# Kernel tuning notes

Measured on AMD Instinct MI355X. Metric: run time of the kernel, lower is better.

## Reference

```python
import jax, jax.numpy as jnp
import numpy as np

COMMITMENT_COST = 0.25


def setup_inputs() -> dict:
    key = jax.random.key(0)
    k1, k2 = jax.random.split(key)
    B, H, W, D, K = 64, 32, 32, 64, 1024
    x = jax.random.normal(k1, (B, H, W, D), dtype=jnp.float32)
    # variance_scaling(fan_in=D, uniform) ~ U(-sqrt(3/D), sqrt(3/D)); plain normal*scale is fine for a reference
    embeddings = jax.random.uniform(k2, (D, K), dtype=jnp.float32,
                                    minval=-np.sqrt(3.0 / D), maxval=np.sqrt(3.0 / D))
    return {"x": x, "embeddings": embeddings}


def reference(x, embeddings):
    D = embeddings.shape[0]
    K = embeddings.shape[1]
    flat = x.reshape(-1, D)                                   # [N, D]
    # squared euclidean distance: ||f||^2 - 2 f.E + ||e||^2 -> [N, K]
    distance = (jnp.sum(flat ** 2, axis=1, keepdims=True)
                - 2.0 * jnp.matmul(flat, embeddings)
                + jnp.sum(embeddings ** 2, axis=0, keepdims=True))
    encoding_indices_flat = jnp.argmax(-distance, axis=1)     # [N]
    encodings = jax.nn.one_hot(encoding_indices_flat, K, dtype=distance.dtype)  # [N, K]
    encoding_indices = encoding_indices_flat.reshape(x.shape[:-1])
    # quantize: gather rows of E^T -> same shape as x
    quantized = jnp.take(embeddings.T, encoding_indices, axis=0)
    e_latent_loss = jnp.mean((jax.lax.stop_gradient(quantized) - x) ** 2)
    q_latent_loss = jnp.mean((quantized - jax.lax.stop_gradient(x)) ** 2)
    loss = q_latent_loss + COMMITMENT_COST * e_latent_loss
    quantized_st = x + jax.lax.stop_gradient(quantized - x)   # straight-through
    avg_probs = jnp.mean(encodings, axis=0)                   # [K]
    perplexity = jnp.exp(-jnp.sum(avg_probs * jnp.log(avg_probs + 1e-10)))
    return quantized_st, loss, perplexity, encoding_indices
```

## Files before the change

### kernel.cpp

```cpp
#include <hip/hip_runtime.h>
#include <math.h>


typedef __attribute__((ext_vector_type(8))) short short8v;
typedef __attribute__((ext_vector_type(4))) float float4v;
typedef unsigned short u16;
typedef unsigned int u32;

constexpr int D = 64;
constexpr int K = 1024;
constexpr int NPTS = 65536;
constexpr long QOFF = (long)NPTS * D;
constexpr float BIAS = 24.0f;
constexpr float GATE = 5e-3f;

constexpr size_t OFF_LOSS = 0;
constexpr size_t OFF_CNT  = 256;
constexpr size_t OFF_EC   = OFF_CNT + 4096;
constexpr size_t OFF_ECB  = OFF_EC + 4096;
constexpr size_t OFF_ET   = OFF_ECB + 4096;
constexpr size_t OFF_STG  = OFF_ET + (size_t)K * D * 4;

__device__ __forceinline__ float med3(float a, float b, float c) {
  return __builtin_amdgcn_fmed3f(a, b, c);
}
__device__ __forceinline__ u16 bf16rtn(float x) {
  u32 u = __float_as_uint(x);
  return (u16)((u + 0x7fffu + ((u >> 16) & 1u)) >> 16);
}
__device__ __forceinline__ float bf2f(u16 h) {
  return __uint_as_float(((u32)h) << 16);
}
__device__ __forceinline__ void gl_lds16(const void* g, void* l) {
  __builtin_amdgcn_global_load_lds(
      (const __attribute__((address_space(1))) u32*)g,
      (__attribute__((address_space(3))) u32*)l, 16, 0, 0);
}

__global__ __launch_bounds__(256) void vq_conv(const float* __restrict__ E,
                                               float* __restrict__ Et,
                                               unsigned char* __restrict__ stg) {
  int gid = blockIdx.x * 256 + threadIdx.x;
  int k = gid & 1023;
  int dg = gid >> 10;
  float v[4];
#pragma unroll
  for (int i = 0; i < 4; ++i) v[i] = E[(dg * 4 + i) * K + k];
  *(float4*)&Et[(size_t)k * 64 + dg * 4] = make_float4(v[0], v[1], v[2], v[3]);
  u16 h[4], l[4];
#pragma unroll
  for (int i = 0; i < 4; ++i) {
    float m2 = -2.0f * v[i];
    h[i] = bf16rtn(m2);
    l[i] = bf16rtn(m2 - bf2f(h[i]));
  }
  int s = dg >> 3, q = (dg >> 1) & 3, jb = (dg & 1) * 4;
  size_t base = (size_t)(k >> 4) * 4096 + (size_t)s * 1024 +
                (size_t)((q * 16 + (k & 15)) * 16) + (size_t)(jb * 2);
  ushort4 hv = {h[0], h[1], h[2], h[3]};
  ushort4 lv = {l[0], l[1], l[2], l[3]};
  *(ushort4*)&stg[base] = hv;
  *(ushort4*)&stg[base + 2048] = lv;
}

__global__ __launch_bounds__(256) void vq_norm(const float* __restrict__ E,
                                               float* __restrict__ eC,
                                               float* __restrict__ eCb,
                                               double* __restrict__ lossSum,
                                               int* __restrict__ counts) {
  int k = blockIdx.x * 256 + threadIdx.x;
  float c = __fmul_rn(E[k], E[k]);
#pragma unroll
  for (int d = 1; d < D; ++d) {
    float vv = E[d * K + k];
    c = __fadd_rn(c, __fmul_rn(vv, vv));
  }
  eC[k] = c;
  eCb[k] = c + BIAS;
  counts[k] = 0;
  if (k == 0) *lossSum = 0.0;
}

__global__ __launch_bounds__(256) void vq_main(const float* __restrict__ x,
                                               const unsigned char* __restrict__ stg,
                                               const float* __restrict__ eC,
                                               const float* __restrict__ eCb,
                                               const float* __restrict__ Etg,
                                               float* __restrict__ out,
                                               double* __restrict__ lossSum,
                                               int* __restrict__ counts) {
  __shared__ __align__(16) unsigned char sbuf[4][2][8192];
  __shared__ __align__(16) float ecb[1024];
  __shared__ __align__(16) float topbuf[256 * 4];
  __shared__ int bkbuf[128];

  const int tid = threadIdx.x;
  const int w = tid >> 6;
  const int lane = tid & 63;
  const int col = lane & 15;
  const int quad = lane >> 4;
  const int blockBase = blockIdx.x * 128;
  const float INF = __builtin_inff();

  *(float4*)&ecb[tid * 4] = *(const float4*)&eCb[tid * 4];

  short8v Bh[2][2], Bl[2][2];
#pragma unroll
  for (int pt = 0; pt < 2; ++pt) {
    const float* xp = x + (size_t)(blockBase + w * 32 + pt * 16 + col) * 64;
#pragma unroll
    for (int s = 0; s < 2; ++s) {
      const float4* src = (const float4*)(xp + s * 32 + quad * 8);
      float4 a = src[0], b = src[1];
      float xs[8] = {a.x, a.y, a.z, a.w, b.x, b.y, b.z, b.w};
      short8v hf, lf;
#pragma unroll
      for (int j = 0; j < 8; ++j) {
        u16 h = bf16rtn(xs[j]);
        hf[j] = (short)h;
        lf[j] = (short)bf16rtn(xs[j] - bf2f(h));
      }
      Bh[pt][s] = hf;
      Bl[pt][s] = lf;
    }
  }

  {
    const unsigned char* s0 = stg + (size_t)lane * 16;
#pragma unroll
    for (int i = 0; i < 8; ++i)
      gl_lds16(s0 + i * 1024, &sbuf[w][0][i * 1024 + lane * 16]);
#pragma unroll
    for (int i = 0; i < 8; ++i)
      gl_lds16(s0 + 8192 + i * 1024, &sbuf[w][1][i * 1024 + lane * 16]);
  }
  asm volatile("s_waitcnt lgkmcnt(0)" ::: "memory");
  __builtin_amdgcn_s_barrier();
  __builtin_amdgcn_sched_barrier(0);
  asm volatile("" ::: "memory");

  float b1[2] = {INF, INF}, b2[2] = {INF, INF};

#pragma unroll 1
  for (int ch = 0; ch < 32; ++ch) {
    const unsigned char* bufB = sbuf[w][ch & 1];
    if (ch < 31) {
      asm volatile("s_waitcnt vmcnt(8)" ::: "memory");
    } else {
      asm volatile("s_waitcnt vmcnt(0)" ::: "memory");
    }
#pragma unroll
    for (int ct2 = 0; ct2 < 2; ++ct2) {
      const unsigned char* fb = bufB + ct2 * 4096 + lane * 16;
      short8v Ah0 = *(const short8v*)(fb);
      short8v Ah1 = *(const short8v*)(fb + 1024);
      short8v Al0 = *(const short8v*)(fb + 2048);
      short8v Al1 = *(const short8v*)(fb + 3072);
      float4v Ci = *(const float4v*)&ecb[ch * 32 + ct2 * 16 + quad * 4];
#pragma unroll
      for (int pt = 0; pt < 2; ++pt) {
        float4v Ca = Ci;
        float4v Cb = {0.f, 0.f, 0.f, 0.f};
        Ca = __builtin_amdgcn_mfma_f32_16x16x32_bf16(Ah0, Bh[pt][0], Ca, 0, 0, 0);
        Cb = __builtin_amdgcn_mfma_f32_16x16x32_bf16(Ah1, Bh[pt][1], Cb, 0, 0, 0);
        Ca = __builtin_amdgcn_mfma_f32_16x16x32_bf16(Al0, Bh[pt][0], Ca, 0, 0, 0);
        Cb = __builtin_amdgcn_mfma_f32_16x16x32_bf16(Al1, Bh[pt][1], Cb, 0, 0, 0);
        Ca = __builtin_amdgcn_mfma_f32_16x16x32_bf16(Ah0, Bl[pt][0], Ca, 0, 0, 0);
        Cb = __builtin_amdgcn_mfma_f32_16x16x32_bf16(Ah1, Bl[pt][1], Cb, 0, 0, 0);
#pragma unroll
        for (int r = 0; r < 4; ++r) {
          float dv = Ca[r] + Cb[r];
          u32 u = (__float_as_uint(dv) & 0xffffff00u) |
                  (u32)(ch * 8 + ct2 * 4 + r);
          float v = __uint_as_float(u);
          float pb = b1[pt];
          b1[pt] = fminf(pb, v);
          b2[pt] = med3(pb, b2[pt], v);
        }
      }
    }
    asm volatile("s_waitcnt lgkmcnt(0)" ::: "memory");
    if (ch < 30) {
      const unsigned char* s2 = stg + (size_t)(ch + 2) * 8192 + (size_t)lane * 16;
#pragma unroll
      for (int i = 0; i < 8; ++i)
        gl_lds16(s2 + i * 1024, &sbuf[w][ch & 1][i * 1024 + lane * 16]);
    }
  }

  topbuf[tid * 4 + 0] = b1[0];
  topbuf[tid * 4 + 1] = b2[0];
  topbuf[tid * 4 + 2] = b1[1];
  topbuf[tid * 4 + 3] = b2[1];
  __syncthreads();

  if (tid < 128) {
    const int mw = tid >> 5, mpt = (tid >> 4) & 1, mcol = tid & 15;
    float cv[8];
    int cq[8];
    float mv0 = INF, mv1 = INF;
    int q0 = 0;
#pragma unroll
    for (int q = 0; q < 4; ++q) {
      int lbase = (mw * 64 + q * 16 + mcol) * 4 + mpt * 2;
#pragma unroll
      for (int j = 0; j < 2; ++j) {
        float v = topbuf[lbase + j];
        cv[q * 2 + j] = v;
        cq[q * 2 + j] = q;
        if (v < mv0) { mv1 = mv0; mv0 = v; q0 = q; }
        else if (v < mv1) { mv1 = v; }
      }
    }
    u32 lb = __float_as_uint(mv0) & 255u;
    int bestk = (int)((lb >> 3) * 32 + ((lb >> 2) & 1) * 16 + q0 * 4 + (lb & 3));

    if (mv1 - mv0 < GATE) {
      const float* f = x + (size_t)(blockBase + tid) * 64;
      float r8[8];
#pragma unroll
      for (int j = 0; j < 8; ++j) { float fv = f[j]; r8[j] = __fmul_rn(fv, fv); }
#pragma unroll
      for (int i = 8; i < D; i += 8)
#pragma unroll
        for (int j = 0; j < 8; ++j) {
          float fv = f[i + j];
          r8[j] = __fadd_rn(r8[j], __fmul_rn(fv, fv));
        }
      float A = __fadd_rn(__fadd_rn(__fadd_rn(r8[0], r8[1]), __fadd_rn(r8[2], r8[3])),
                          __fadd_rn(__fadd_rn(r8[4], r8[5]), __fadd_rn(r8[6], r8[7])));
      float bd = INF;
      int bkk = K;
#pragma unroll
      for (int c = 0; c < 8; ++c) {
        u32 cb = __float_as_uint(cv[c]) & 255u;
        int k = (int)((cb >> 3) * 32 + ((cb >> 2) & 1) * 16 + cq[c] * 4 + (cb & 3));
        const float* er = Etg + (size_t)k * 64;
        float m = 0.f;
#pragma unroll
        for (int d = 0; d < D; ++d) m = __fmaf_rn(f[d], er[d], m);
        float dist = __fadd_rn(__fsub_rn(A, __fmul_rn(2.f, m)), eC[k]);
        bool better = (dist < bd) || (dist == bd && k < bkk);
        bd = better ? dist : bd;
        bkk = better ? k : bkk;
      }
      bestk = bkk;
    }

    bkbuf[tid] = bestk;
    out[QOFF + 2 + blockBase + tid] = (float)bestk;
    atomicAdd(&counts[bestk], 1);
  }
  __syncthreads();

  const int pp = tid >> 1, half = tid & 1;
  const int bk = bkbuf[pp];
  const float4* et = (const float4*)(Etg + (size_t)bk * 64 + half * 32);
  const float4* xr = (const float4*)(x + (size_t)(blockBase + pp) * 64 + half * 32);
  float4* ov = (float4*)(out + (size_t)(blockBase + pp) * 64 + half * 32);
  float errs = 0.f;
#pragma unroll
  for (int i = 0; i < 8; ++i) {
    float4 qv = et[i];
    float4 xv = xr[i];
    float dx;
    dx = qv.x - xv.x; errs = fmaf(dx, dx, errs);
    dx = qv.y - xv.y; errs = fmaf(dx, dx, errs);
    dx = qv.z - xv.z; errs = fmaf(dx, dx, errs);
    dx = qv.w - xv.w; errs = fmaf(dx, dx, errs);
    ov[i] = qv;
  }
  double de = (double)errs;
#pragma unroll
  for (int off = 32; off > 0; off >>= 1) de += __shfl_down(de, off, 64);
  if (lane == 0) atomicAdd(lossSum, de);
}

__global__ __launch_bounds__(256) void vq_finalize(const double* __restrict__ lossSum,
                                                   const int* __restrict__ counts,
                                                   float* __restrict__ out) {
  __shared__ double sh[256];
  double ent = 0.0;
  for (int k = threadIdx.x; k < K; k += 256) {
    double pp = (double)counts[k] / (double)NPTS;
    ent += pp * log(pp + 1e-10);
  }
  sh[threadIdx.x] = ent;
  __syncthreads();
  for (int s = 128; s > 0; s >>= 1) {
    if (threadIdx.x < s) sh[threadIdx.x] += sh[threadIdx.x + s];
    __syncthreads();
  }
  if (threadIdx.x == 0) {
    out[QOFF + 0] = (float)(1.25 * (*lossSum) / (double)((long)NPTS * D));
    out[QOFF + 1] = (float)exp(-sh[0]);
  }
}

extern "C" void kernel_launch(void* const* d_in, const int* in_sizes, int n_in,
                              void* d_out, int out_size, void* d_ws, size_t ws_size,
                              hipStream_t stream) {
  const float* x = (const float*)d_in[0];
  const float* E = (const float*)d_in[1];
  float* out = (float*)d_out;

  char* ws = (char*)d_ws;
  double* lossSum = (double*)(ws + OFF_LOSS);
  int* counts = (int*)(ws + OFF_CNT);
  float* eC = (float*)(ws + OFF_EC);
  float* eCb = (float*)(ws + OFF_ECB);
  float* Etg = (float*)(ws + OFF_ET);
  unsigned char* stgb = (unsigned char*)(ws + OFF_STG);

  vq_conv<<<64, 256, 0, stream>>>(E, Etg, stgb);
  vq_norm<<<4, 256, 0, stream>>>(E, eC, eCb, lossSum, counts);
  vq_main<<<NPTS / 128, 256, 0, stream>>>(x, stgb, eC, eCb, Etg, out,
                                          lossSum, counts);
  vq_finalize<<<1, 256, 0, stream>>>(lossSum, counts, out);
}
```

Measured before the change: 130.4 us.

## Halve points per wave and codebook chunk size to raise occupancy

Each wave now handles 16 points instead of 32, and each staged codebook chunk holds 16 codes (4 KB) instead of 32, so the loop runs 64 iterations instead of 32. The grid doubles to 1024 blocks, LDS per block shrinks, and launch_bounds requests 4 blocks per CU. The aim is more resident waves and better latency hiding. In exchange, every staged codebook chunk is reused across half as many points, so total global/LDS traffic for the codebook doubles and there are more loop iterations and waits per MFMA.

```diff
diff --git a/kernel.cpp b/kernel.cpp
--- a/kernel.cpp
+++ b/kernel.cpp
@@ -81,33 +81,32 @@
   if (k == 0) *lossSum = 0.0;
 }
 
-__global__ __launch_bounds__(256) void vq_main(const float* __restrict__ x,
-                                               const unsigned char* __restrict__ stg,
-                                               const float* __restrict__ eC,
-                                               const float* __restrict__ eCb,
-                                               const float* __restrict__ Etg,
-                                               float* __restrict__ out,
-                                               double* __restrict__ lossSum,
-                                               int* __restrict__ counts) {
-  __shared__ __align__(16) unsigned char sbuf[4][2][8192];
+__global__ __launch_bounds__(256, 4) void vq_main(const float* __restrict__ x,
+                                                  const unsigned char* __restrict__ stg,
+                                                  const float* __restrict__ eC,
+                                                  const float* __restrict__ eCb,
+                                                  const float* __restrict__ Etg,
+                                                  float* __restrict__ out,
+                                                  double* __restrict__ lossSum,
+                                                  int* __restrict__ counts) {
+  __shared__ __align__(16) unsigned char sbuf[4][2][4096];
   __shared__ __align__(16) float ecb[1024];
-  __shared__ __align__(16) float topbuf[256 * 4];
-  __shared__ int bkbuf[128];
+  __shared__ __align__(16) float topbuf[256 * 2];
+  __shared__ int bkbuf[64];
 
   const int tid = threadIdx.x;
   const int w = tid >> 6;
   const int lane = tid & 63;
   const int col = lane & 15;
   const int quad = lane >> 4;
-  const int blockBase = blockIdx.x * 128;
+  const int blockBase = blockIdx.x * 64;
   const float INF = __builtin_inff();
 
   *(float4*)&ecb[tid * 4] = *(const float4*)&eCb[tid * 4];
 
-  short8v Bh[2][2], Bl[2][2];
-#pragma unroll
-  for (int pt = 0; pt < 2; ++pt) {
-    const float* xp = x + (size_t)(blockBase + w * 32 + pt * 16 + col) * 64;
+  short8v Bh[2], Bl[2];
+  {
+    const float* xp = x + (size_t)(blockBase + w * 16 + col) * 64;
 #pragma unroll
     for (int s = 0; s < 2; ++s) {
       const float4* src = (const float4*)(xp + s * 32 + quad * 8);
@@ -120,89 +119,80 @@
         hf[j] = (short)h;
         lf[j] = (short)bf16rtn(xs[j] - bf2f(h));
       }
-      Bh[pt][s] = hf;
-      Bl[pt][s] = lf;
+      Bh[s] = hf;
+      Bl[s] = lf;
     }
   }
 
   {
     const unsigned char* s0 = stg + (size_t)lane * 16;
 #pragma unroll
-    for (int i = 0; i < 8; ++i)
+    for (int i = 0; i < 4; ++i)
       gl_lds16(s0 + i * 1024, &sbuf[w][0][i * 1024 + lane * 16]);
 #pragma unroll
-    for (int i = 0; i < 8; ++i)
-      gl_lds16(s0 + 8192 + i * 1024, &sbuf[w][1][i * 1024 + lane * 16]);
+    for (int i = 0; i < 4; ++i)
+      gl_lds16(s0 + 4096 + i * 1024, &sbuf[w][1][i * 1024 + lane * 16]);
   }
   asm volatile("s_waitcnt lgkmcnt(0)" ::: "memory");
   __builtin_amdgcn_s_barrier();
   __builtin_amdgcn_sched_barrier(0);
   asm volatile("" ::: "memory");
 
-  float b1[2] = {INF, INF}, b2[2] = {INF, INF};
+  float b1 = INF, b2 = INF;
 
 #pragma unroll 1
-  for (int ch = 0; ch < 32; ++ch) {
+  for (int ch = 0; ch < 64; ++ch) {
     const unsigned char* bufB = sbuf[w][ch & 1];
-    if (ch < 31) {
-      asm volatile("s_waitcnt vmcnt(8)" ::: "memory");
+    if (ch < 63) {
+      asm volatile("s_waitcnt vmcnt(4)" ::: "memory");
     } else {
       asm volatile("s_waitcnt vmcnt(0)" ::: "memory");
     }
-#pragma unroll
-    for (int ct2 = 0; ct2 < 2; ++ct2) {
-      const unsigned char* fb = bufB + ct2 * 4096 + lane * 16;
-      short8v Ah0 = *(const short8v*)(fb);
-      short8v Ah1 = *(const short8v*)(fb + 1024);
-      short8v Al0 = *(const short8v*)(fb + 2048);
-      short8v Al1 = *(const short8v*)(fb + 3072);
-      float4v Ci = *(const float4v*)&ecb[ch * 32 + ct2 * 16 + quad * 4];
-#pragma unroll
-      for (int pt = 0; pt < 2; ++pt) {
-        float4v Ca = Ci;
-        float4v Cb = {0.f, 0.f, 0.f, 0.f};
-        Ca = __builtin_amdgcn_mfma_f32_16x16x32_bf16(Ah0, Bh[pt][0], Ca, 0, 0, 0);
-        Cb = __builtin_amdgcn_mfma_f32_16x16x32_bf16(Ah1, Bh[pt][1], Cb, 0, 0, 0);
-        Ca = __builtin_amdgcn_mfma_f32_16x16x32_bf16(Al0, Bh[pt][0], Ca, 0, 0, 0);
-        Cb = __builtin_amdgcn_mfma_f32_16x16x32_bf16(Al1, Bh[pt][1], Cb, 0, 0, 0);
-        Ca = __builtin_amdgcn_mfma_f32_16x16x32_bf16(Ah0, Bl[pt][0], Ca, 0, 0, 0);
-        Cb = __builtin_amdgcn_mfma_f32_16x16x32_bf16(Ah1, Bl[pt][1], Cb, 0, 0, 0);
-#pragma unroll
-        for (int r = 0; r < 4; ++r) {
-          float dv = Ca[r] + Cb[r];
-          u32 u = (__float_as_uint(dv) & 0xffffff00u) |
-                  (u32)(ch * 8 + ct2 * 4 + r);
-          float v = __uint_as_float(u);
-          float pb = b1[pt];
-          b1[pt] = fminf(pb, v);
-          b2[pt] = med3(pb, b2[pt], v);
-        }
-      }
+    const unsigned char* fb = bufB + lane * 16;
+    short8v Ah0 = *(const short8v*)(fb);
+    short8v Ah1 = *(const short8v*)(fb + 1024);
+    short8v Al0 = *(const short8v*)(fb + 2048);
+    short8v Al1 = *(const short8v*)(fb + 3072);
+    float4v Ci = *(const float4v*)&ecb[ch * 16 + quad * 4];
+    float4v Ca = Ci;
+    float4v Cb = {0.f, 0.f, 0.f, 0.f};
+    Ca = __builtin_amdgcn_mfma_f32_16x16x32_bf16(Ah0, Bh[0], Ca, 0, 0, 0);
+    Cb = __builtin_amdgcn_mfma_f32_16x16x32_bf16(Ah1, Bh[1], Cb, 0, 0, 0);
+    Ca = __builtin_amdgcn_mfma_f32_16x16x32_bf16(Al0, Bh[0], Ca, 0, 0, 0);
+    Cb = __builtin_amdgcn_mfma_f32_16x16x32_bf16(Al1, Bh[1], Cb, 0, 0, 0);
+    Ca = __builtin_amdgcn_mfma_f32_16x16x32_bf16(Ah0, Bl[0], Ca, 0, 0, 0);
+    Cb = __builtin_amdgcn_mfma_f32_16x16x32_bf16(Ah1, Bl[1], Cb, 0, 0, 0);
+#pragma unroll
+    for (int r = 0; r < 4; ++r) {
+      float dv = Ca[r] + Cb[r];
+      u32 u = (__float_as_uint(dv) & 0xffffff00u) | (u32)(ch * 4 + r);
+      float v = __uint_as_float(u);
+      float pb = b1;
+      b1 = fminf(pb, v);
+      b2 = med3(pb, b2, v);
     }
     asm volatile("s_waitcnt lgkmcnt(0)" ::: "memory");
-    if (ch < 30) {
-      const unsigned char* s2 = stg + (size_t)(ch + 2) * 8192 + (size_t)lane * 16;
-#pragma unroll
-      for (int i = 0; i < 8; ++i)
+    if (ch < 62) {
+      const unsigned char* s2 = stg + (size_t)(ch + 2) * 4096 + (size_t)lane * 16;
+#pragma unroll
+      for (int i = 0; i < 4; ++i)
         gl_lds16(s2 + i * 1024, &sbuf[w][ch & 1][i * 1024 + lane * 16]);
     }
   }
 
-  topbuf[tid * 4 + 0] = b1[0];
-  topbuf[tid * 4 + 1] = b2[0];
-  topbuf[tid * 4 + 2] = b1[1];
-  topbuf[tid * 4 + 3] = b2[1];
+  topbuf[tid * 2 + 0] = b1;
+  topbuf[tid * 2 + 1] = b2;
   __syncthreads();
 
-  if (tid < 128) {
-    const int mw = tid >> 5, mpt = (tid >> 4) & 1, mcol = tid & 15;
+  if (tid < 64) {
+    const int mpt = tid >> 4, mcol = tid & 15;
     float cv[8];
     int cq[8];
     float mv0 = INF, mv1 = INF;
     int q0 = 0;
 #pragma unroll
     for (int q = 0; q < 4; ++q) {
-      int lbase = (mw * 64 + q * 16 + mcol) * 4 + mpt * 2;
+      int lbase = (mpt * 64 + q * 16 + mcol) * 2;
 #pragma unroll
       for (int j = 0; j < 2; ++j) {
         float v = topbuf[lbase + j];
@@ -213,7 +203,7 @@
       }
     }
     u32 lb = __float_as_uint(mv0) & 255u;
-    int bestk = (int)((lb >> 3) * 32 + ((lb >> 2) & 1) * 16 + q0 * 4 + (lb & 3));
+    int bestk = (int)((lb >> 2) * 16 + q0 * 4 + (lb & 3));
 
     if (mv1 - mv0 < GATE) {
       const float* f = x + (size_t)(blockBase + tid) * 64;
@@ -234,7 +224,7 @@
 #pragma unroll
       for (int c = 0; c < 8; ++c) {
         u32 cb = __float_as_uint(cv[c]) & 255u;
-        int k = (int)((cb >> 3) * 32 + ((cb >> 2) & 1) * 16 + cq[c] * 4 + (cb & 3));
+        int k = (int)((cb >> 2) * 16 + cq[c] * 4 + (cb & 3));
         const float* er = Etg + (size_t)k * 64;
         float m = 0.f;
 #pragma unroll
@@ -253,14 +243,14 @@
   }
   __syncthreads();
 
-  const int pp = tid >> 1, half = tid & 1;
+  const int pp = tid >> 2, qtr = tid & 3;
   const int bk = bkbuf[pp];
-  const float4* et = (const float4*)(Etg + (size_t)bk * 64 + half * 32);
-  const float4* xr = (const float4*)(x + (size_t)(blockBase + pp) * 64 + half * 32);
-  float4* ov = (float4*)(out + (size_t)(blockBase + pp) * 64 + half * 32);
+  const float4* et = (const float4*)(Etg + (size_t)bk * 64 + qtr * 16);
+  const float4* xr = (const float4*)(x + (size_t)(blockBase + pp) * 64 + qtr * 16);
+  float4* ov = (float4*)(out + (size_t)(blockBase + pp) * 64 + qtr * 16);
   float errs = 0.f;
 #pragma unroll
-  for (int i = 0; i < 8; ++i) {
+  for (int i = 0; i < 4; ++i) {
     float4 qv = et[i];
     float4 xv = xr[i];
     float dx;
@@ -314,7 +304,7 @@
 
   vq_conv<<<64, 256, 0, stream>>>(E, Etg, stgb);
   vq_norm<<<4, 256, 0, stream>>>(E, eC, eCb, lossSum, counts);
-  vq_main<<<NPTS / 128, 256, 0, stream>>>(x, stgb, eC, eCb, Etg, out,
-                                          lossSum, counts);
+  vq_main<<<NPTS / 64, 256, 0, stream>>>(x, stgb, eC, eCb, Etg, out,
+                                         lossSum, counts);
   vq_finalize<<<1, 256, 0, stream>>>(lossSum, counts, out);
 }
```

Result: slower. 161.5 us (+23.9%).
